# Kernel tuning notes

Hardware: AMD Instinct MI355X
Metric: run time of the kernel (lower is better)

The kernel has to match this reference:

```python
import jax, jax.numpy as jnp
import numpy as np

N_PER_G = 18
GRAPHS = 4096
N = GRAPHS * N_PER_G            # 73728 nodes
E = GRAPHS * N_PER_G * (N_PER_G - 1)  # 1253376 edges (fully connected per graph)
F_IN = 1536                     # sfreq * timestep
EPS = 1e-5
SLOPE = 0.01


def _lrelu(v):
    return jnp.where(v >= 0, v, SLOPE * v)


def setup_inputs() -> dict:
    key = jax.random.key(0)
    ks = jax.random.split(key, 32)
    # node features
    x = jax.random.normal(ks[0], (N, F_IN), dtype=jnp.float32)
    # fully-connected edges within each 18-node graph
    src, dst = np.meshgrid(np.arange(N_PER_G), np.arange(N_PER_G), indexing='ij')
    m = src != dst
    src, dst = src[m], dst[m]                      # [306]
    offs = (np.arange(GRAPHS) * N_PER_G)[:, None]
    row = (offs + src[None, :]).reshape(-1)
    col = (offs + dst[None, :]).reshape(-1)
    edge_index = jnp.asarray(np.stack([row, col]), dtype=jnp.int32)  # [2,E]
    edge_weight = jax.random.uniform(ks[1], (E,), dtype=jnp.float32)
    batch = jnp.asarray(np.arange(N) // N_PER_G, dtype=jnp.int32)

    def lin(k, fi, fo):
        kw, kb = jax.random.split(k)
        s = 1.0 / np.sqrt(fi)
        W = jax.random.uniform(kw, (fi, fo), jnp.float32, -s, s)
        b = jax.random.uniform(kb, (fo,), jnp.float32, -s, s)
        return W, b

    def bn(k, f):
        k1, k2 = jax.random.split(k)
        g = jnp.ones((f,), jnp.float32)
        be = jnp.zeros((f,), jnp.float32)
        rm = jax.random.normal(k1, (f,), jnp.float32) * 0.1
        rv = jax.random.uniform(k2, (f,), jnp.float32) + 0.5
        return g, be, rm, rv

    W1, b1 = lin(ks[2], F_IN, 32)
    W2, b2 = lin(ks[3], 32, 64)
    W3, b3 = lin(ks[4], 64, 128)
    g1, be1, rm1, rv1 = bn(ks[5], 32)
    g2, be2, rm2, rv2 = bn(ks[6], 64)
    g3, be3, rm3, rv3 = bn(ks[7], 128)
    fW1, fb1 = lin(ks[8], 128, 64)
    fW2, fb2 = lin(ks[9], 64, 32)
    fW3, fb3 = lin(ks[10], 32, 16)
    fW4, fb4 = lin(ks[11], 16, 1)

    return dict(x=x, edge_index=edge_index, edge_weight=edge_weight, batch=batch,
                W1=W1, b1=b1, g1=g1, be1=be1, rm1=rm1, rv1=rv1,
                W2=W2, b2=b2, g2=g2, be2=be2, rm2=rm2, rv2=rv2,
                W3=W3, b3=b3, g3=g3, be3=be3, rm3=rm3, rv3=rv3,
                fW1=fW1, fb1=fb1, fW2=fW2, fb2=fb2,
                fW3=fW3, fb3=fb3, fW4=fW4, fb4=fb4)


def _gcn_norm(edge_index, edge_weight):
    # add self loops (weight 1), symmetric normalization (PyG GCNConv, improved=False)
    row = jnp.concatenate([edge_index[0], jnp.arange(N, dtype=edge_index.dtype)])
    col = jnp.concatenate([edge_index[1], jnp.arange(N, dtype=edge_index.dtype)])
    w = jnp.concatenate([edge_weight, jnp.ones((N,), edge_weight.dtype)])
    deg = jax.ops.segment_sum(w, col, num_segments=N)
    dinv = jnp.where(deg > 0, jax.lax.rsqrt(jnp.maximum(deg, 1e-30)), 0.0)
    norm = dinv[row] * w * dinv[col]
    return row, col, norm


def _gcn(x, W, b, row, col, norm):
    h = x @ W                                       # [N, Fout]
    out = jax.ops.segment_sum(norm[:, None] * h[row], col, num_segments=N)
    return out + b


def _bn(h, g, be, rm, rv):
    return (h - rm) * jax.lax.rsqrt(rv + EPS) * g + be


def reference(x, edge_index, edge_weight, batch,
              W1, b1, g1, be1, rm1, rv1,
              W2, b2, g2, be2, rm2, rv2,
              W3, b3, g3, be3, rm3, rv3,
              fW1, fb1, fW2, fb2, fW3, fb3, fW4, fb4):
    row, col, norm = _gcn_norm(edge_index, edge_weight)
    h = _lrelu(_bn(_gcn(x, W1, b1, row, col, norm), g1, be1, rm1, rv1))
    h = _lrelu(_bn(_gcn(h, W2, b2, row, col, norm), g2, be2, rm2, rv2))
    h = _lrelu(_bn(_gcn(h, W3, b3, row, col, norm), g3, be3, rm3, rv3))
    # global mean pool over graphs
    sums = jax.ops.segment_sum(h, batch, num_segments=GRAPHS)
    cnt = jax.ops.segment_sum(jnp.ones((N,), h.dtype), batch, num_segments=GRAPHS)
    h = sums / jnp.maximum(cnt, 1.0)[:, None]       # [G,128]
    # MLP head (dropout = identity in eval)
    h = _lrelu(h @ fW1 + fb1)
    h = _lrelu(h @ fW2 + fb2)
    h = _lrelu(h @ fW3 + fb3)
    h = h @ fW4 + fb4
    return h.squeeze(-1)                            # [G]
```

## Files before the change

kernel.cpp:

```cpp
#include <hip/hip_runtime.h>
#include <stdint.h>

#define GRAPHS 4096
#define NPG 18
#define EPERG 306
#define FIN 1536
#define BN_EPS 1e-5f
#define SLOPE 0.01f

using short8  = __attribute__((ext_vector_type(8))) short;
using ushort8 = __attribute__((ext_vector_type(8))) unsigned short;
using f32x4   = __attribute__((ext_vector_type(4))) float;

__device__ __forceinline__ unsigned short f2bf(float f) {
  unsigned u = __builtin_bit_cast(unsigned, f);
  u += 0x7fffu + ((u >> 16) & 1u);
  return (unsigned short)(u >> 16);
}

__global__ void prep_kernel(const float* __restrict__ W1,
    const float* __restrict__ b1, const float* __restrict__ g1,
    const float* __restrict__ be1, const float* __restrict__ rm1, const float* __restrict__ rv1,
    const float* __restrict__ b2, const float* __restrict__ g2,
    const float* __restrict__ be2, const float* __restrict__ rm2, const float* __restrict__ rv2,
    const float* __restrict__ b3, const float* __restrict__ g3,
    const float* __restrict__ be3, const float* __restrict__ rm3, const float* __restrict__ rv3,
    unsigned short* __restrict__ w1frag, float* __restrict__ ab) {
  const int tid = threadIdx.x;
  if (blockIdx.x < 24) {
    int slot = blockIdx.x * 256 + tid;
    int L  = slot & 63;
    int nt = (slot >> 6) & 1;
    int ks = slot >> 7;
    int n  = nt * 16 + (L & 15);
    int kb = ks * 32 + ((L >> 4) << 3);
    ushort8 v;
#pragma unroll
    for (int j = 0; j < 8; ++j) v[j] = f2bf(W1[(kb + j) * 32 + n]);
    *((ushort8*)w1frag + slot) = v;
  } else {
    if (tid < 32) {
      float a = g1[tid] * rsqrtf(rv1[tid] + BN_EPS);
      ab[tid] = a; ab[32 + tid] = (b1[tid] - rm1[tid]) * a + be1[tid];
    }
    if (tid < 64) {
      float a = g2[tid] * rsqrtf(rv2[tid] + BN_EPS);
      ab[64 + tid] = a; ab[128 + tid] = (b2[tid] - rm2[tid]) * a + be2[tid];
    }
    if (tid < 128) {
      float a = g3[tid] * rsqrtf(rv3[tid] + BN_EPS);
      ab[192 + tid] = a; ab[320 + tid] = (b3[tid] - rm3[tid]) * a + be3[tid];
    }
  }
}

__global__ __launch_bounds__(256, 4) void gcn_main(
    const float* __restrict__ x, const float* __restrict__ ew,
    const float* __restrict__ W2, const float* __restrict__ W3,
    const float* __restrict__ fW1, const float* __restrict__ fb1,
    const float* __restrict__ fW2, const float* __restrict__ fb2,
    const float* __restrict__ fW3, const float* __restrict__ fb3,
    const float* __restrict__ fW4, const float* __restrict__ fb4,
    const unsigned short* __restrict__ w1frag, const float* __restrict__ ab,
    float* __restrict__ out) {
  const int g    = blockIdx.x;
  const int tid  = threadIdx.x;
  const int lane = tid & 63;
  const int wv   = tid >> 6;

  __shared__ float ew_s[EPERG];
  __shared__ float dinv_s[NPG];
  __shared__ float An[NPG][NPG + 1];
  __shared__ short xA[32][136];
  __shared__ float Pb[NPG][129];
  __shared__ float Hb[NPG][129];
  __shared__ float pooled[128];
  __shared__ float m1[64];
  __shared__ float m2[32];
  __shared__ float m3[16];

  for (int i = tid; i < EPERG; i += 256) ew_s[i] = ew[g * EPERG + i];
  for (int i = tid; i < 14 * 68; i += 256) {
    int r = 18 + i / 68, c = i % 68;
    ((int*)&xA[r][0])[c] = 0;
  }
  __syncthreads();

  if (tid < NPG) {
    float deg = 1.0f;
#pragma unroll
    for (int j = 0; j < 17; ++j) {
      int s = j + (j >= tid);
      deg += ew_s[s * 17 + (tid - (tid > s ? 1 : 0))];
    }
    dinv_s[tid] = rsqrtf(deg);
  }
  __syncthreads();

  for (int o = tid; o < NPG * NPG; o += 256) {
    int d = o / NPG, s = o - d * NPG;
    float v;
    if (d == s) v = dinv_s[d] * dinv_s[d];
    else        v = dinv_s[s] * ew_s[s * 17 + (d - (d > s ? 1 : 0))] * dinv_s[d];
    An[d][s] = v;
  }

  const int Mt = wv & 1, Nt = wv >> 1;
  const int arow  = Mt * 16 + (lane & 15);
  const int akoff = (lane >> 4) << 3;
  f32x4 acc = {0.f, 0.f, 0.f, 0.f};
  const float4* __restrict__ x4 = (const float4*)x + (size_t)g * 18 * 384;

  for (int c = 0; c < 12; ++c) {
    const int k0d4 = c * 32;
    for (int idx = tid; idx < 576; idx += 256) {
      int r = idx >> 5, c4 = idx & 31;
      float4 v = x4[r * 384 + k0d4 + c4];
      ushort4 b;
      b.x = f2bf(v.x); b.y = f2bf(v.y); b.z = f2bf(v.z); b.w = f2bf(v.w);
      *(ushort4*)(&xA[r][c4 * 4]) = b;
    }
    __syncthreads();
#pragma unroll
    for (int kk = 0; kk < 4; ++kk) {
      short8 af = *(const short8*)(&xA[arow][kk * 32 + akoff]);
      short8 bf = *(const short8*)(w1frag + (size_t)(((c * 4 + kk) * 2 + Nt) * 64 + lane) * 8);
      acc = __builtin_amdgcn_mfma_f32_16x16x32_bf16(af, bf, acc, 0, 0, 0);
    }
    __syncthreads();
  }

  {
    int ccol  = Nt * 16 + (lane & 15);
    int rbase = Mt * 16 + ((lane >> 4) << 2);
#pragma unroll
    for (int q = 0; q < 4; ++q) {
      int rr = rbase + q;
      if (rr < NPG) Pb[rr][ccol] = acc[q];
    }
  }
  __syncthreads();

  for (int o = tid; o < NPG * 32; o += 256) {
    int d = o >> 5, cc = o & 31;
    float s = 0.f;
#pragma unroll
    for (int ss = 0; ss < NPG; ++ss) s = fmaf(An[d][ss], Pb[ss][cc], s);
    float v = fmaf(s, ab[cc], ab[32 + cc]);
    Hb[d][cc] = v >= 0.f ? v : SLOPE * v;
  }
  __syncthreads();

  for (int o = tid; o < NPG * 64; o += 256) {
    int r = o >> 6, cc = o & 63;
    float s = 0.f;
#pragma unroll
    for (int k = 0; k < 32; ++k) s = fmaf(Hb[r][k], W2[k * 64 + cc], s);
    Pb[r][cc] = s;
  }
  __syncthreads();
  for (int o = tid; o < NPG * 64; o += 256) {
    int d = o >> 6, cc = o & 63;
    float s = 0.f;
#pragma unroll
    for (int ss = 0; ss < NPG; ++ss) s = fmaf(An[d][ss], Pb[ss][cc], s);
    float v = fmaf(s, ab[64 + cc], ab[128 + cc]);
    Hb[d][cc] = v >= 0.f ? v : SLOPE * v;
  }
  __syncthreads();

  for (int o = tid; o < NPG * 128; o += 256) {
    int r = o >> 7, cc = o & 127;
    float s = 0.f;
#pragma unroll
    for (int k = 0; k < 64; ++k) s = fmaf(Hb[r][k], W3[k * 128 + cc], s);
    Pb[r][cc] = s;
  }
  __syncthreads();
  for (int o = tid; o < NPG * 128; o += 256) {
    int d = o >> 7, cc = o & 127;
    float s = 0.f;
#pragma unroll
    for (int ss = 0; ss < NPG; ++ss) s = fmaf(An[d][ss], Pb[ss][cc], s);
    float v = fmaf(s, ab[192 + cc], ab[320 + cc]);
    Hb[d][cc] = v >= 0.f ? v : SLOPE * v;
  }
  __syncthreads();

  if (tid < 128) {
    float s = 0.f;
#pragma unroll
    for (int d = 0; d < NPG; ++d) s += Hb[d][tid];
    pooled[tid] = s * (1.0f / 18.0f);
  }
  __syncthreads();
  if (tid < 64) {
    float s = fb1[tid];
#pragma unroll 8
    for (int k = 0; k < 128; ++k) s = fmaf(pooled[k], fW1[k * 64 + tid], s);
    m1[tid] = s >= 0.f ? s : SLOPE * s;
  }
  __syncthreads();
  if (tid < 32) {
    float s = fb2[tid];
#pragma unroll
    for (int k = 0; k < 64; ++k) s = fmaf(m1[k], fW2[k * 32 + tid], s);
    m2[tid] = s >= 0.f ? s : SLOPE * s;
  }
  __syncthreads();
  if (tid < 16) {
    float s = fb3[tid];
#pragma unroll
    for (int k = 0; k < 32; ++k) s = fmaf(m2[k], fW3[k * 16 + tid], s);
    m3[tid] = s >= 0.f ? s : SLOPE * s;
  }
  __syncthreads();
  if (tid == 0) {
    float s = fb4[0];
#pragma unroll
    for (int k = 0; k < 16; ++k) s = fmaf(m3[k], fW4[k], s);
    out[g] = s;
  }
}

extern "C" void kernel_launch(void* const* d_in, const int* in_sizes, int n_in,
                              void* d_out, int out_size, void* d_ws, size_t ws_size,
                              hipStream_t stream) {
  const float* x   = (const float*)d_in[0];
  const float* ew  = (const float*)d_in[2];
  const float* W1  = (const float*)d_in[4];
  const float* b1  = (const float*)d_in[5];
  const float* g1  = (const float*)d_in[6];
  const float* be1 = (const float*)d_in[7];
  const float* rm1 = (const float*)d_in[8];
  const float* rv1 = (const float*)d_in[9];
  const float* W2  = (const float*)d_in[10];
  const float* b2  = (const float*)d_in[11];
  const float* g2  = (const float*)d_in[12];
  const float* be2 = (const float*)d_in[13];
  const float* rm2 = (const float*)d_in[14];
  const float* rv2 = (const float*)d_in[15];
  const float* W3  = (const float*)d_in[16];
  const float* b3  = (const float*)d_in[17];
  const float* g3  = (const float*)d_in[18];
  const float* be3 = (const float*)d_in[19];
  const float* rm3 = (const float*)d_in[20];
  const float* rv3 = (const float*)d_in[21];
  const float* fW1 = (const float*)d_in[22];
  const float* fb1 = (const float*)d_in[23];
  const float* fW2 = (const float*)d_in[24];
  const float* fb2 = (const float*)d_in[25];
  const float* fW3 = (const float*)d_in[26];
  const float* fb3 = (const float*)d_in[27];
  const float* fW4 = (const float*)d_in[28];
  const float* fb4 = (const float*)d_in[29];

  unsigned short* w1frag = (unsigned short*)d_ws;
  float* ab = (float*)((char*)d_ws + 98304);

  prep_kernel<<<25, 256, 0, stream>>>(W1, b1, g1, be1, rm1, rv1,
                                      b2, g2, be2, rm2, rv2,
                                      b3, g3, be3, rm3, rv3, w1frag, ab);
  gcn_main<<<GRAPHS, 256, 0, stream>>>(x, ew, W2, W3, fW1, fb1, fW2, fb2,
                                       fW3, fb3, fW4, fb4, w1frag, ab,
                                       (float*)d_out);
}
```

Before: 729.0 us.

## Double-buffer x tiles with register prefetch and vectorize per-graph GCN layers

The first-layer loop now prefetches the next 32-column x chunk into registers while converting and storing the current one into one of two LDS buffers. This drops one barrier per iteration and hides global-load latency. The small dense layers are rewritten so each thread computes four output columns with float4 loads, and the staging buffer shares LDS with the projection buffer through a union. The risks are higher register pressure under the 4-blocks-per-SM launch bound and LDS races if the union reuse is mis-synchronised.

```diff
diff --git a/kernel.cpp b/kernel.cpp
--- a/kernel.cpp
+++ b/kernel.cpp
@@ -54,6 +54,11 @@
   }
 }
 
+union SmemU {
+  short xA[2][32][136];
+  float Pb[NPG][132];
+};
+
 __global__ __launch_bounds__(256, 4) void gcn_main(
     const float* __restrict__ x, const float* __restrict__ ew,
     const float* __restrict__ W2, const float* __restrict__ W3,
@@ -71,18 +76,18 @@
   __shared__ float ew_s[EPERG];
   __shared__ float dinv_s[NPG];
   __shared__ float An[NPG][NPG + 1];
-  __shared__ short xA[32][136];
-  __shared__ float Pb[NPG][129];
-  __shared__ float Hb[NPG][129];
+  __shared__ SmemU u;
+  __shared__ float Hb[NPG][132];
   __shared__ float pooled[128];
   __shared__ float m1[64];
   __shared__ float m2[32];
   __shared__ float m3[16];
 
   for (int i = tid; i < EPERG; i += 256) ew_s[i] = ew[g * EPERG + i];
-  for (int i = tid; i < 14 * 68; i += 256) {
-    int r = 18 + i / 68, c = i % 68;
-    ((int*)&xA[r][0])[c] = 0;
+  for (int i = tid; i < 2 * 14 * 68; i += 256) {
+    int b = i / 952, rem = i - b * 952;
+    int r = 18 + rem / 68, c = rem - (rem / 68) * 68;
+    ((int*)&u.xA[b][r][0])[c] = 0;
   }
   __syncthreads();
 
@@ -111,24 +116,48 @@
   f32x4 acc = {0.f, 0.f, 0.f, 0.f};
   const float4* __restrict__ x4 = (const float4*)x + (size_t)g * 18 * 384;
 
+  float4 cur[3], nxt[3];
+#pragma unroll
+  for (int i = 0; i < 3; ++i) {
+    int idx = tid + i * 256;
+    if (idx < 576) { int r = idx >> 5, c4 = idx & 31; cur[i] = x4[r * 384 + c4]; }
+  }
+
   for (int c = 0; c < 12; ++c) {
-    const int k0d4 = c * 32;
-    for (int idx = tid; idx < 576; idx += 256) {
-      int r = idx >> 5, c4 = idx & 31;
-      float4 v = x4[r * 384 + k0d4 + c4];
-      ushort4 b;
-      b.x = f2bf(v.x); b.y = f2bf(v.y); b.z = f2bf(v.z); b.w = f2bf(v.w);
-      *(ushort4*)(&xA[r][c4 * 4]) = b;
+    if (c < 11) {
+#pragma unroll
+      for (int i = 0; i < 3; ++i) {
+        int idx = tid + i * 256;
+        if (idx < 576) { int r = idx >> 5, c4 = idx & 31; nxt[i] = x4[r * 384 + (c + 1) * 32 + c4]; }
+      }
+    }
+    short8 bf[4];
+#pragma unroll
+    for (int kk = 0; kk < 4; ++kk)
+      bf[kk] = *(const short8*)(w1frag + (size_t)(((c * 4 + kk) * 2 + Nt) * 64 + lane) * 8);
+
+    short (*xb)[136] = u.xA[c & 1];
+#pragma unroll
+    for (int i = 0; i < 3; ++i) {
+      int idx = tid + i * 256;
+      if (idx < 576) {
+        int r = idx >> 5, c4 = idx & 31;
+        ushort4 b;
+        b.x = f2bf(cur[i].x); b.y = f2bf(cur[i].y);
+        b.z = f2bf(cur[i].z); b.w = f2bf(cur[i].w);
+        *(ushort4*)(&xb[r][c4 * 4]) = b;
+      }
     }
     __syncthreads();
 #pragma unroll
     for (int kk = 0; kk < 4; ++kk) {
-      short8 af = *(const short8*)(&xA[arow][kk * 32 + akoff]);
-      short8 bf = *(const short8*)(w1frag + (size_t)(((c * 4 + kk) * 2 + Nt) * 64 + lane) * 8);
-      acc = __builtin_amdgcn_mfma_f32_16x16x32_bf16(af, bf, acc, 0, 0, 0);
-    }
-    __syncthreads();
-  }
+      short8 af = *(const short8*)(&xb[arow][kk * 32 + akoff]);
+      acc = __builtin_amdgcn_mfma_f32_16x16x32_bf16(af, bf[kk], acc, 0, 0, 0);
+    }
+#pragma unroll
+    for (int i = 0; i < 3; ++i) cur[i] = nxt[i];
+  }
+  __syncthreads();
 
   {
     int ccol  = Nt * 16 + (lane & 15);
@@ -136,54 +165,94 @@
 #pragma unroll
     for (int q = 0; q < 4; ++q) {
       int rr = rbase + q;
-      if (rr < NPG) Pb[rr][ccol] = acc[q];
+      if (rr < NPG) u.Pb[rr][ccol] = acc[q];
+    }
+  }
+  __syncthreads();
+
+  if (tid < NPG * 8) {
+    int d = tid >> 3, c4 = tid & 7;
+    f32x4 s = {0.f, 0.f, 0.f, 0.f};
+#pragma unroll
+    for (int ss = 0; ss < NPG; ++ss) {
+      float a = An[d][ss];
+      const f32x4 p = *(const f32x4*)&u.Pb[ss][c4 * 4];
+#pragma unroll
+      for (int j = 0; j < 4; ++j) s[j] = fmaf(a, p[j], s[j]);
+    }
+    const f32x4 al = *(const f32x4*)(ab + c4 * 4);
+    const f32x4 bt = *(const f32x4*)(ab + 32 + c4 * 4);
+#pragma unroll
+    for (int j = 0; j < 4; ++j) {
+      float v = fmaf(s[j], al[j], bt[j]);
+      Hb[d][c4 * 4 + j] = v >= 0.f ? v : SLOPE * v;
+    }
+  }
+  __syncthreads();
+
+  for (int o = tid; o < NPG * 16; o += 256) {
+    int r = o >> 4, c4 = o & 15;
+    f32x4 s = {0.f, 0.f, 0.f, 0.f};
+#pragma unroll 8
+    for (int k = 0; k < 32; ++k) {
+      float h = Hb[r][k];
+      const f32x4 w = *(const f32x4*)&W2[k * 64 + c4 * 4];
+#pragma unroll
+      for (int j = 0; j < 4; ++j) s[j] = fmaf(h, w[j], s[j]);
+    }
+    *(f32x4*)&u.Pb[r][c4 * 4] = s;
+  }
+  __syncthreads();
+  for (int o = tid; o < NPG * 16; o += 256) {
+    int d = o >> 4, c4 = o & 15;
+    f32x4 s = {0.f, 0.f, 0.f, 0.f};
+#pragma unroll
+    for (int ss = 0; ss < NPG; ++ss) {
+      float a = An[d][ss];
+      const f32x4 p = *(const f32x4*)&u.Pb[ss][c4 * 4];
+#pragma unroll
+      for (int j = 0; j < 4; ++j) s[j] = fmaf(a, p[j], s[j]);
+    }
+    const f32x4 al = *(const f32x4*)(ab + 64 + c4 * 4);
+    const f32x4 bt = *(const f32x4*)(ab + 128 + c4 * 4);
+#pragma unroll
+    for (int j = 0; j < 4; ++j) {
+      float v = fmaf(s[j], al[j], bt[j]);
+      Hb[d][c4 * 4 + j] = v >= 0.f ? v : SLOPE * v;
     }
   }
   __syncthreads();
 
   for (int o = tid; o < NPG * 32; o += 256) {
-    int d = o >> 5, cc = o & 31;
-    float s = 0.f;
-#pragma unroll
-    for (int ss = 0; ss < NPG; ++ss) s = fmaf(An[d][ss], Pb[ss][cc], s);
-    float v = fmaf(s, ab[cc], ab[32 + cc]);
-    Hb[d][cc] = v >= 0.f ? v : SLOPE * v;
-  }
-  __syncthreads();
-
-  for (int o = tid; o < NPG * 64; o += 256) {
-    int r = o >> 6, cc = o & 63;
-    float s = 0.f;
-#pragma unroll
-    for (int k = 0; k < 32; ++k) s = fmaf(Hb[r][k], W2[k * 64 + cc], s);
-    Pb[r][cc] = s;
-  }
-  __syncthreads();
-  for (int o = tid; o < NPG * 64; o += 256) {
-    int d = o >> 6, cc = o & 63;
-    float s = 0.f;
-#pragma unroll
-    for (int ss = 0; ss < NPG; ++ss) s = fmaf(An[d][ss], Pb[ss][cc], s);
-    float v = fmaf(s, ab[64 + cc], ab[128 + cc]);
-    Hb[d][cc] = v >= 0.f ? v : SLOPE * v;
-  }
-  __syncthreads();
-
-  for (int o = tid; o < NPG * 128; o += 256) {
-    int r = o >> 7, cc = o & 127;
-    float s = 0.f;
-#pragma unroll
-    for (int k = 0; k < 64; ++k) s = fmaf(Hb[r][k], W3[k * 128 + cc], s);
-    Pb[r][cc] = s;
-  }
-  __syncthreads();
-  for (int o = tid; o < NPG * 128; o += 256) {
-    int d = o >> 7, cc = o & 127;
-    float s = 0.f;
-#pragma unroll
-    for (int ss = 0; ss < NPG; ++ss) s = fmaf(An[d][ss], Pb[ss][cc], s);
-    float v = fmaf(s, ab[192 + cc], ab[320 + cc]);
-    Hb[d][cc] = v >= 0.f ? v : SLOPE * v;
+    int r = o >> 5, c4 = o & 31;
+    f32x4 s = {0.f, 0.f, 0.f, 0.f};
+#pragma unroll 8
+    for (int k = 0; k < 64; ++k) {
+      float h = Hb[r][k];
+      const f32x4 w = *(const f32x4*)&W3[k * 128 + c4 * 4];
+#pragma unroll
+      for (int j = 0; j < 4; ++j) s[j] = fmaf(h, w[j], s[j]);
+    }
+    *(f32x4*)&u.Pb[r][c4 * 4] = s;
+  }
+  __syncthreads();
+  for (int o = tid; o < NPG * 32; o += 256) {
+    int d = o >> 5, c4 = o & 31;
+    f32x4 s = {0.f, 0.f, 0.f, 0.f};
+#pragma unroll
+    for (int ss = 0; ss < NPG; ++ss) {
+      float a = An[d][ss];
+      const f32x4 p = *(const f32x4*)&u.Pb[ss][c4 * 4];
+#pragma unroll
+      for (int j = 0; j < 4; ++j) s[j] = fmaf(a, p[j], s[j]);
+    }
+    const f32x4 al = *(const f32x4*)(ab + 192 + c4 * 4);
+    const f32x4 bt = *(const f32x4*)(ab + 320 + c4 * 4);
+#pragma unroll
+    for (int j = 0; j < 4; ++j) {
+      float v = fmaf(s[j], al[j], bt[j]);
+      Hb[d][c4 * 4 + j] = v >= 0.f ? v : SLOPE * v;
+    }
   }
   __syncthreads();
 
@@ -226,6 +295,7 @@
 extern "C" void kernel_launch(void* const* d_in, const int* in_sizes, int n_in,
                               void* d_out, int out_size, void* d_ws, size_t ws_size,
                               hipStream_t stream) {
+  (void)in_sizes; (void)n_in; (void)out_size; (void)ws_size;
   const float* x   = (const float*)d_in[0];
   const float* ew  = (const float*)d_in[2];
   const float* W1  = (const float*)d_in[4];
```

Measured after the change: 747.0 us. +2.5%, slower.
